# Kernel optimization log

Hardware: AMD Instinct MI355X
Metric: run time of the kernel (lower is better)

Reference implementation:

```python
import jax, jax.numpy as jnp
import numpy as np

VOL_SHAPE = (160, 192, 160)

def setup_inputs() -> dict:
    key = jax.random.key(0)
    k1, k2 = jax.random.split(key)
    vol = jax.random.normal(k1, (2, *VOL_SHAPE, 1), dtype=jnp.float32)
    trf = jax.random.normal(k2, (2, *VOL_SHAPE, 3), dtype=jnp.float32)
    return {"vol": vol, "trf": trf}

def _warp(vol, trf):
    # vol: [B, X, Y, Z, C]; trf: [B, X, Y, Z, 3] dense displacement field ('ij' indexing)
    B = vol.shape[0]
    shape = vol.shape[1:-1]
    nd = len(shape)
    # sample locations = identity grid + displacement
    grid = jnp.stack(jnp.meshgrid(*[jnp.arange(s, dtype=vol.dtype) for s in shape], indexing='ij'), axis=-1)
    loc = grid[None] + trf  # [B, X, Y, Z, 3]
    max_f = jnp.array([s - 1 for s in shape], dtype=vol.dtype)
    max_i = jnp.array([s - 1 for s in shape], dtype=jnp.int32)
    # fill_value=None -> clamp to volume border (voxelmorph interpn semantics)
    loc = jnp.clip(loc, 0.0, max_f)
    loc0f = jnp.floor(loc)
    loc0 = jnp.clip(loc0f.astype(jnp.int32), 0, max_i)        # lower corner indices
    loc1 = jnp.clip(loc0 + 1, 0, max_i)                       # upper corner indices (clipped)
    d1 = loc1.astype(vol.dtype) - loc                          # weight for lower corner
    d0 = 1.0 - d1                                              # weight for upper corner
    b = jnp.arange(B)[:, None, None, None]
    out = jnp.zeros(vol.shape, dtype=vol.dtype)
    for c in range(2 ** nd):                                   # 8 corners, fixed small loop
        bits = [(c >> d) & 1 for d in range(nd)]
        idx = [loc1[..., d] if bits[d] else loc0[..., d] for d in range(nd)]
        w = jnp.ones(loc.shape[:-1], dtype=vol.dtype)
        for d in range(nd):
            w = w * (d0[..., d] if bits[d] else d1[..., d])
        out = out + w[..., None] * vol[b, idx[0], idx[1], idx[2]]
    return out

def reference(vol, trf):
    return _warp(vol, trf)
```

## Files before the change

### kernel.cpp

```cpp
#include <hip/hip_runtime.h>


#define NXD 160
#define NYD 192
#define NZD 160
#define NVOX (NXD * NYD * NZD)
#define NBATCH 2

#define TXT 8
#define TYT 16
#define TZT 16
#define LXT 14
#define LYT 22
#define LZT 32
#define NROWS (LXT * LYT)
#define LDS_N (NROWS * LZT)
#define NSLOT (NROWS * 8)

#define TILES_X (NXD / TXT)
#define TILES_Y (NYD / TYT)
#define TILES_Z (NZD / TZT)
#define NBLOCKS (NBATCH * TILES_X * TILES_Y * TILES_Z)

typedef float f4 __attribute__((ext_vector_type(4)));

__global__ __launch_bounds__(512)
void warp3d_kernel(const float* __restrict__ vol,
                   const float* __restrict__ trf,
                   float* __restrict__ out) {
    __shared__ float tile[LDS_N];

    int bid0 = blockIdx.x;
    int bid = (bid0 & 7) * (NBLOCKS / 8) + (bid0 >> 3);

    int tz = bid % TILES_Z;
    int r  = bid / TILES_Z;
    int ty = r % TILES_Y;
    int r2 = r / TILES_Y;
    int tx = r2 % TILES_X;
    int b  = r2 / TILES_X;

    int x0t = tx * TXT, y0t = ty * TYT, z0t = tz * TZT;
    int lox = min(max(x0t - 3, 0), NXD - LXT);
    int loy = min(max(y0t - 3, 0), NYD - LYT);
    int loz = min(max(z0t - 8, 0), NZD - LZT);

    const float* vb = vol + (size_t)b * NVOX;

    int t = threadIdx.x;
    int zq = t & 3;
    int yq = (t >> 2) & 15;
    int xq = t >> 6;
    int x = x0t + xq, y = y0t + yq, zb0 = z0t + zq * 4;
    size_t vox_i = (((size_t)b * NXD + x) * NYD + y) * NZD + zb0;

    const f4* trfv = (const f4*)(trf + vox_i * 3);
    f4 t0 = trfv[0], t1 = trfv[1], t2 = trfv[2];

    {
        const float* gbase = vb + ((size_t)(lox * NYD + loy) * NZD + loz);
#pragma unroll
        for (int it = 0; it < 5; ++it) {
            int slot = it * 512 + t;
            if (slot < NSLOT) {
                int row = slot >> 3;
                int zg  = (slot & 7) << 2;
                int yi  = row % LYT;
                int xi  = row / LYT;
                int sz  = zg ^ ((yi & 7) << 2);
                const float* g = gbase + (size_t)xi * (NYD * NZD) + yi * NZD + sz;
                __builtin_amdgcn_global_load_lds(
                    (const __attribute__((address_space(1))) void*)g,
                    (__attribute__((address_space(3))) void*)&tile[slot * 4],
                    16, 0, 0);
            }
        }
    }
    __syncthreads();

    float dxa[4] = {t0.x, t0.w, t1.z, t2.y};
    float dya[4] = {t0.y, t1.x, t1.w, t2.z};
    float dza[4] = {t0.z, t1.y, t2.x, t2.w};

    float res[4];
#pragma unroll
    for (int j = 0; j < 4; ++j) {
        float lx = fminf(fmaxf((float)x + dxa[j], 0.0f), (float)(NXD - 1));
        float ly = fminf(fmaxf((float)y + dya[j], 0.0f), (float)(NYD - 1));
        float lz = fminf(fmaxf((float)(zb0 + j) + dza[j], 0.0f), (float)(NZD - 1));
        float fx = floorf(lx), fy = floorf(ly), fz = floorf(lz);
        int x0 = (int)fx, y0 = (int)fy, z0 = (int)fz;
        float wx0 = fminf(fx + 1.0f, (float)(NXD - 1)) - lx;
        float wy0 = fminf(fy + 1.0f, (float)(NYD - 1)) - ly;
        float wz0 = fminf(fz + 1.0f, (float)(NZD - 1)) - lz;

        int ix = x0 - lox, iy = y0 - loy, iz = z0 - loz;
        bool ok = ((unsigned)ix <= LXT - 2) & ((unsigned)iy <= LYT - 2) &
                  ((unsigned)iz <= LZT - 2);
        int sx = ok ? ix : 0;
        int sy = ok ? iy : 0;
        int sv = ok ? iz : 0;

        int base = (sx * LYT + sy) * LZT;
        int sw0 = (sy & 7) << 2;
        int sw1 = ((sy + 1) & 7) << 2;
        int A = base + (sv ^ sw0);
        int B = base + ((sv + 1) ^ sw0);
        int C = base + LZT + (sv ^ sw1);
        int D = base + LZT + ((sv + 1) ^ sw1);

        float v000 = tile[A],              v001 = tile[B];
        float v010 = tile[C],              v011 = tile[D];
        float v100 = tile[A + LYT * LZT],  v101 = tile[B + LYT * LZT];
        float v110 = tile[C + LYT * LZT],  v111 = tile[D + LYT * LZT];

        if (!ok) {
            int x1 = min(x0 + 1, NXD - 1);
            int y1 = min(y0 + 1, NYD - 1);
            int z1 = min(z0 + 1, NZD - 1);
            size_t o00 = (size_t)(x0 * NYD + y0) * NZD;
            size_t o01 = (size_t)(x0 * NYD + y1) * NZD;
            size_t o10 = (size_t)(x1 * NYD + y0) * NZD;
            size_t o11 = (size_t)(x1 * NYD + y1) * NZD;
            v000 = vb[o00 + z0]; v001 = vb[o00 + z1];
            v010 = vb[o01 + z0]; v011 = vb[o01 + z1];
            v100 = vb[o10 + z0]; v101 = vb[o10 + z1];
            v110 = vb[o11 + z0]; v111 = vb[o11 + z1];
        }

        float wx1 = 1.0f - wx0, wy1 = 1.0f - wy0, wz1 = 1.0f - wz0;
        res[j] = wx0 * (wy0 * (wz0 * v000 + wz1 * v001) +
                        wy1 * (wz0 * v010 + wz1 * v011)) +
                 wx1 * (wy0 * (wz0 * v100 + wz1 * v101) +
                        wy1 * (wz0 * v110 + wz1 * v111));
    }

    f4 o;
    o.x = res[0]; o.y = res[1]; o.z = res[2]; o.w = res[3];
    *(f4*)(out + vox_i) = o;
}

extern "C" void kernel_launch(void* const* d_in, const int* in_sizes, int n_in,
                              void* d_out, int out_size, void* d_ws, size_t ws_size,
                              hipStream_t stream) {
    const float* vol = (const float*)d_in[0];
    const float* trf = (const float*)d_in[1];
    float* out = (float*)d_out;

    warp3d_kernel<<<NBLOCKS, 512, 0, stream>>>(vol, trf, out);
}
```

Measured before the change: 222.1 us.

## Make blocks persistent along z with double-buffered LDS tile prefetch

Each block now walks all z tiles of its x-y column instead of handling one tile, and prefetches the next z halo tile and displacement vectors into a second LDS buffer while interpolating the current one. This is meant to hide global-to-LDS load latency behind compute and cut per-block launch and setup overhead. In exchange, LDS use per block doubles, there are ten times fewer blocks, which reduces parallelism and occupancy, and the z tiles of a column are processed serially.

```diff
diff --git a/kernel.cpp b/kernel.cpp
--- a/kernel.cpp
+++ b/kernel.cpp
@@ -10,6 +10,7 @@
 #define TXT 8
 #define TYT 16
 #define TZT 16
+#define NZT (NZD / TZT)
 #define LXT 14
 #define LYT 22
 #define LZT 32
@@ -19,31 +20,30 @@
 
 #define TILES_X (NXD / TXT)
 #define TILES_Y (NYD / TYT)
-#define TILES_Z (NZD / TZT)
-#define NBLOCKS (NBATCH * TILES_X * TILES_Y * TILES_Z)
+#define NBLOCKS (NBATCH * TILES_X * TILES_Y)
 
 typedef float f4 __attribute__((ext_vector_type(4)));
+
+#define AS1 __attribute__((address_space(1)))
+#define AS3 __attribute__((address_space(3)))
 
 __global__ __launch_bounds__(512)
 void warp3d_kernel(const float* __restrict__ vol,
                    const float* __restrict__ trf,
                    float* __restrict__ out) {
-    __shared__ float tile[LDS_N];
+    __shared__ float tile[2 * LDS_N];
 
     int bid0 = blockIdx.x;
     int bid = (bid0 & 7) * (NBLOCKS / 8) + (bid0 >> 3);
 
-    int tz = bid % TILES_Z;
-    int r  = bid / TILES_Z;
-    int ty = r % TILES_Y;
-    int r2 = r / TILES_Y;
-    int tx = r2 % TILES_X;
-    int b  = r2 / TILES_X;
+    int ty = bid % TILES_Y;
+    int r  = bid / TILES_Y;
+    int tx = r % TILES_X;
+    int b  = r / TILES_X;
 
-    int x0t = tx * TXT, y0t = ty * TYT, z0t = tz * TZT;
+    int x0t = tx * TXT, y0t = ty * TYT;
     int lox = min(max(x0t - 3, 0), NXD - LXT);
     int loy = min(max(y0t - 3, 0), NYD - LYT);
-    int loz = min(max(z0t - 8, 0), NZD - LZT);
 
     const float* vb = vol + (size_t)b * NVOX;
 
@@ -51,93 +51,130 @@
     int zq = t & 3;
     int yq = (t >> 2) & 15;
     int xq = t >> 6;
-    int x = x0t + xq, y = y0t + yq, zb0 = z0t + zq * 4;
-    size_t vox_i = (((size_t)b * NXD + x) * NYD + y) * NZD + zb0;
+    int x = x0t + xq, y = y0t + yq;
+    size_t rowb = (((size_t)b * NXD + x) * NYD + y) * NZD + zq * 4;
 
-    const f4* trfv = (const f4*)(trf + vox_i * 3);
-    f4 t0 = trfv[0], t1 = trfv[1], t2 = trfv[2];
+    int o0, o1, o2, o3, o4;
+    {
+#define MKOFF(IT, DST)                                                    \
+        {                                                                  \
+            int slot = (IT) * 512 + t;                                     \
+            int row = slot >> 3;                                           \
+            int zg  = (slot & 7) << 2;                                     \
+            int yi  = row % LYT;                                           \
+            int xi  = row / LYT;                                           \
+            int sz  = zg ^ ((yi & 7) << 2);   \
+            DST = xi * (NYD * NZD) + yi * NZD + sz;                        \
+        }
+        MKOFF(0, o0) MKOFF(1, o1) MKOFF(2, o2) MKOFF(3, o3) MKOFF(4, o4)
+#undef MKOFF
+    }
+    bool p4 = (2048 + t) < NSLOT;
 
+    auto STAGE = [&](int bufoff, int loz) {
+        const float* gb = vb + ((size_t)(lox * NYD + loy) * NZD + loz);
+        __builtin_amdgcn_global_load_lds((const AS1 void*)(gb + o0),
+            (AS3 void*)&tile[bufoff + t * 4], 16, 0, 0);
+        __builtin_amdgcn_global_load_lds((const AS1 void*)(gb + o1),
+            (AS3 void*)&tile[bufoff + (512 + t) * 4], 16, 0, 0);
+        __builtin_amdgcn_global_load_lds((const AS1 void*)(gb + o2),
+            (AS3 void*)&tile[bufoff + (1024 + t) * 4], 16, 0, 0);
+        __builtin_amdgcn_global_load_lds((const AS1 void*)(gb + o3),
+            (AS3 void*)&tile[bufoff + (1536 + t) * 4], 16, 0, 0);
+        if (p4)
+            __builtin_amdgcn_global_load_lds((const AS1 void*)(gb + o4),
+                (AS3 void*)&tile[bufoff + (2048 + t) * 4], 16, 0, 0);
+    };
+
+    int bufoff = 0;
+    int loz = 0;
+    f4 ta0, ta1, ta2;
     {
-        const float* gbase = vb + ((size_t)(lox * NYD + loy) * NZD + loz);
+        const f4* tv = (const f4*)(trf + rowb * 3);
+        ta0 = tv[0]; ta1 = tv[1]; ta2 = tv[2];
+    }
+    STAGE(0, 0);
+    __syncthreads();
+
+    for (int tz = 0; tz < NZT; ++tz) {
+        bool pre = (tz + 1) < NZT;
+        int loz_next = min(max((tz + 1) * TZT - 8, 0), NZD - LZT);
+        f4 tb0, tb1, tb2;
+        if (pre) {
+            const f4* tv = (const f4*)(trf + (rowb + (size_t)(tz + 1) * TZT) * 3);
+            tb0 = tv[0]; tb1 = tv[1]; tb2 = tv[2];
+            STAGE(bufoff ^ LDS_N, loz_next);
+        }
+
+        int zb0 = tz * TZT + zq * 4;
+        float dxa[4] = {ta0.x, ta0.w, ta1.z, ta2.y};
+        float dya[4] = {ta0.y, ta1.x, ta1.w, ta2.z};
+        float dza[4] = {ta0.z, ta1.y, ta2.x, ta2.w};
+
+        float res[4];
 #pragma unroll
-        for (int it = 0; it < 5; ++it) {
-            int slot = it * 512 + t;
-            if (slot < NSLOT) {
-                int row = slot >> 3;
-                int zg  = (slot & 7) << 2;
-                int yi  = row % LYT;
-                int xi  = row / LYT;
-                int sz  = zg ^ ((yi & 7) << 2);
-                const float* g = gbase + (size_t)xi * (NYD * NZD) + yi * NZD + sz;
-                __builtin_amdgcn_global_load_lds(
-                    (const __attribute__((address_space(1))) void*)g,
-                    (__attribute__((address_space(3))) void*)&tile[slot * 4],
-                    16, 0, 0);
+        for (int j = 0; j < 4; ++j) {
+            float lx = fminf(fmaxf((float)x + dxa[j], 0.0f), (float)(NXD - 1));
+            float ly = fminf(fmaxf((float)y + dya[j], 0.0f), (float)(NYD - 1));
+            float lz = fminf(fmaxf((float)(zb0 + j) + dza[j], 0.0f), (float)(NZD - 1));
+            float fx = floorf(lx), fy = floorf(ly), fz = floorf(lz);
+            int x0 = (int)fx, y0 = (int)fy, z0 = (int)fz;
+            float wx0 = fminf(fx + 1.0f, (float)(NXD - 1)) - lx;
+            float wy0 = fminf(fy + 1.0f, (float)(NYD - 1)) - ly;
+            float wz0 = fminf(fz + 1.0f, (float)(NZD - 1)) - lz;
+
+            int ix = x0 - lox, iy = y0 - loy, iz = z0 - loz;
+            bool ok = ((unsigned)ix <= LXT - 2) & ((unsigned)iy <= LYT - 2) &
+                      ((unsigned)iz <= LZT - 2);
+            int sx = ok ? ix : 0;
+            int sy = ok ? iy : 0;
+            int sv = ok ? iz : 0;
+
+            int base = bufoff + (sx * LYT + sy) * LZT;
+            int sw0 = (sy & 7) << 2;
+            int sw1 = ((sy + 1) & 7) << 2;
+            int A = base + (sv ^ sw0);
+            int B = base + ((sv + 1) ^ sw0);
+            int C = base + LZT + (sv ^ sw1);
+            int D = base + LZT + ((sv + 1) ^ sw1);
+
+            float v000 = tile[A],              v001 = tile[B];
+            float v010 = tile[C],              v011 = tile[D];
+            float v100 = tile[A + LYT * LZT],  v101 = tile[B + LYT * LZT];
+            float v110 = tile[C + LYT * LZT],  v111 = tile[D + LYT * LZT];
+
+            if (!ok) {
+                int x1 = min(x0 + 1, NXD - 1);
+                int y1 = min(y0 + 1, NYD - 1);
+                int z1 = min(z0 + 1, NZD - 1);
+                size_t o00 = (size_t)(x0 * NYD + y0) * NZD;
+                size_t o01 = (size_t)(x0 * NYD + y1) * NZD;
+                size_t o10 = (size_t)(x1 * NYD + y0) * NZD;
+                size_t o11 = (size_t)(x1 * NYD + y1) * NZD;
+                v000 = vb[o00 + z0]; v001 = vb[o00 + z1];
+                v010 = vb[o01 + z0]; v011 = vb[o01 + z1];
+                v100 = vb[o10 + z0]; v101 = vb[o10 + z1];
+                v110 = vb[o11 + z0]; v111 = vb[o11 + z1];
             }
+
+            float wx1 = 1.0f - wx0, wy1 = 1.0f - wy0, wz1 = 1.0f - wz0;
+            res[j] = wx0 * (wy0 * (wz0 * v000 + wz1 * v001) +
+                            wy1 * (wz0 * v010 + wz1 * v011)) +
+                     wx1 * (wy0 * (wz0 * v100 + wz1 * v101) +
+                            wy1 * (wz0 * v110 + wz1 * v111));
+        }
+
+        f4 o;
+        o.x = res[0]; o.y = res[1]; o.z = res[2]; o.w = res[3];
+        *(f4*)(out + rowb + (size_t)tz * TZT) = o;
+
+        __syncthreads();
+        if (pre) {
+            ta0 = tb0; ta1 = tb1; ta2 = tb2;
+            bufoff ^= LDS_N;
+            loz = loz_next;
         }
     }
-    __syncthreads();
-
-    float dxa[4] = {t0.x, t0.w, t1.z, t2.y};
-    float dya[4] = {t0.y, t1.x, t1.w, t2.z};
-    float dza[4] = {t0.z, t1.y, t2.x, t2.w};
-
-    float res[4];
-#pragma unroll
-    for (int j = 0; j < 4; ++j) {
-        float lx = fminf(fmaxf((float)x + dxa[j], 0.0f), (float)(NXD - 1));
-        float ly = fminf(fmaxf((float)y + dya[j], 0.0f), (float)(NYD - 1));
-        float lz = fminf(fmaxf((float)(zb0 + j) + dza[j], 0.0f), (float)(NZD - 1));
-        float fx = floorf(lx), fy = floorf(ly), fz = floorf(lz);
-        int x0 = (int)fx, y0 = (int)fy, z0 = (int)fz;
-        float wx0 = fminf(fx + 1.0f, (float)(NXD - 1)) - lx;
-        float wy0 = fminf(fy + 1.0f, (float)(NYD - 1)) - ly;
-        float wz0 = fminf(fz + 1.0f, (float)(NZD - 1)) - lz;
-
-        int ix = x0 - lox, iy = y0 - loy, iz = z0 - loz;
-        bool ok = ((unsigned)ix <= LXT - 2) & ((unsigned)iy <= LYT - 2) &
-                  ((unsigned)iz <= LZT - 2);
-        int sx = ok ? ix : 0;
-        int sy = ok ? iy : 0;
-        int sv = ok ? iz : 0;
-
-        int base = (sx * LYT + sy) * LZT;
-        int sw0 = (sy & 7) << 2;
-        int sw1 = ((sy + 1) & 7) << 2;
-        int A = base + (sv ^ sw0);
-        int B = base + ((sv + 1) ^ sw0);
-        int C = base + LZT + (sv ^ sw1);
-        int D = base + LZT + ((sv + 1) ^ sw1);
-
-        float v000 = tile[A],              v001 = tile[B];
-        float v010 = tile[C],              v011 = tile[D];
-        float v100 = tile[A + LYT * LZT],  v101 = tile[B + LYT * LZT];
-        float v110 = tile[C + LYT * LZT],  v111 = tile[D + LYT * LZT];
-
-        if (!ok) {
-            int x1 = min(x0 + 1, NXD - 1);
-            int y1 = min(y0 + 1, NYD - 1);
-            int z1 = min(z0 + 1, NZD - 1);
-            size_t o00 = (size_t)(x0 * NYD + y0) * NZD;
-            size_t o01 = (size_t)(x0 * NYD + y1) * NZD;
-            size_t o10 = (size_t)(x1 * NYD + y0) * NZD;
-            size_t o11 = (size_t)(x1 * NYD + y1) * NZD;
-            v000 = vb[o00 + z0]; v001 = vb[o00 + z1];
-            v010 = vb[o01 + z0]; v011 = vb[o01 + z1];
-            v100 = vb[o10 + z0]; v101 = vb[o10 + z1];
-            v110 = vb[o11 + z0]; v111 = vb[o11 + z1];
-        }
-
-        float wx1 = 1.0f - wx0, wy1 = 1.0f - wy0, wz1 = 1.0f - wz0;
-        res[j] = wx0 * (wy0 * (wz0 * v000 + wz1 * v001) +
-                        wy1 * (wz0 * v010 + wz1 * v011)) +
-                 wx1 * (wy0 * (wz0 * v100 + wz1 * v101) +
-                        wy1 * (wz0 * v110 + wz1 * v111));
-    }
-
-    f4 o;
-    o.x = res[0]; o.y = res[1]; o.z = res[2]; o.w = res[3];
-    *(f4*)(out + vox_i) = o;
 }
 
 extern "C" void kernel_launch(void* const* d_in, const int* in_sizes, int n_in,
```

New measurement: 239.0 us. 7.6% more time.

## Replace LDS tile staging with direct global gathers per voxel

Applied to the files above, without the earlier changes.

Drops the shared-memory halo tile, the async global-to-LDS copy and the block barrier. Each thread now gathers all eight trilinear corners straight from global memory and relies on the L1/L2 caches for reuse. Blocks shrink to 256 threads over a flat linear voxel-quad index. This removes the halo overfetch and the barrier stall, at the cost of many more scattered global load instructions going through the cache hierarchy.

```diff
diff --git a/kernel.cpp b/kernel.cpp
--- a/kernel.cpp
+++ b/kernel.cpp
@@ -7,76 +7,34 @@
 #define NVOX (NXD * NYD * NZD)
 #define NBATCH 2
 
-#define TXT 8
-#define TYT 16
-#define TZT 16
-#define LXT 14
-#define LYT 22
-#define LZT 32
-#define NROWS (LXT * LYT)
-#define LDS_N (NROWS * LZT)
-#define NSLOT (NROWS * 8)
-
-#define TILES_X (NXD / TXT)
-#define TILES_Y (NYD / TYT)
-#define TILES_Z (NZD / TZT)
-#define NBLOCKS (NBATCH * TILES_X * TILES_Y * TILES_Z)
+#define ZQ (NZD / 4)
+#define NQUAD (NBATCH * NXD * NYD * ZQ)
+#define BLK 256
+#define NBLOCKS (NQUAD / BLK)
 
 typedef float f4 __attribute__((ext_vector_type(4)));
 
-__global__ __launch_bounds__(512)
+__global__ __launch_bounds__(BLK)
 void warp3d_kernel(const float* __restrict__ vol,
                    const float* __restrict__ trf,
                    float* __restrict__ out) {
-    __shared__ float tile[LDS_N];
-
     int bid0 = blockIdx.x;
     int bid = (bid0 & 7) * (NBLOCKS / 8) + (bid0 >> 3);
 
-    int tz = bid % TILES_Z;
-    int r  = bid / TILES_Z;
-    int ty = r % TILES_Y;
-    int r2 = r / TILES_Y;
-    int tx = r2 % TILES_X;
-    int b  = r2 / TILES_X;
+    int q = bid * BLK + threadIdx.x;
+    int zqi = q % ZQ;
+    int r   = q / ZQ;
+    int y   = r % NYD;
+    int r2  = r / NYD;
+    int x   = r2 % NXD;
+    int b   = r2 / NXD;
 
-    int x0t = tx * TXT, y0t = ty * TYT, z0t = tz * TZT;
-    int lox = min(max(x0t - 3, 0), NXD - LXT);
-    int loy = min(max(y0t - 3, 0), NYD - LYT);
-    int loz = min(max(z0t - 8, 0), NZD - LZT);
-
+    int zb0 = zqi * 4;
+    size_t rowb = (((size_t)b * NXD + x) * NYD + y) * NZD + zb0;
     const float* vb = vol + (size_t)b * NVOX;
 
-    int t = threadIdx.x;
-    int zq = t & 3;
-    int yq = (t >> 2) & 15;
-    int xq = t >> 6;
-    int x = x0t + xq, y = y0t + yq, zb0 = z0t + zq * 4;
-    size_t vox_i = (((size_t)b * NXD + x) * NYD + y) * NZD + zb0;
-
-    const f4* trfv = (const f4*)(trf + vox_i * 3);
-    f4 t0 = trfv[0], t1 = trfv[1], t2 = trfv[2];
-
-    {
-        const float* gbase = vb + ((size_t)(lox * NYD + loy) * NZD + loz);
-#pragma unroll
-        for (int it = 0; it < 5; ++it) {
-            int slot = it * 512 + t;
-            if (slot < NSLOT) {
-                int row = slot >> 3;
-                int zg  = (slot & 7) << 2;
-                int yi  = row % LYT;
-                int xi  = row / LYT;
-                int sz  = zg ^ ((yi & 7) << 2);
-                const float* g = gbase + (size_t)xi * (NYD * NZD) + yi * NZD + sz;
-                __builtin_amdgcn_global_load_lds(
-                    (const __attribute__((address_space(1))) void*)g,
-                    (__attribute__((address_space(3))) void*)&tile[slot * 4],
-                    16, 0, 0);
-            }
-        }
-    }
-    __syncthreads();
+    const f4* tv = (const f4*)(trf + rowb * 3);
+    f4 t0 = tv[0], t1 = tv[1], t2 = tv[2];
 
     float dxa[4] = {t0.x, t0.w, t1.z, t2.y};
     float dya[4] = {t0.y, t1.x, t1.w, t2.z};
@@ -94,39 +52,18 @@
         float wy0 = fminf(fy + 1.0f, (float)(NYD - 1)) - ly;
         float wz0 = fminf(fz + 1.0f, (float)(NZD - 1)) - lz;
 
-        int ix = x0 - lox, iy = y0 - loy, iz = z0 - loz;
-        bool ok = ((unsigned)ix <= LXT - 2) & ((unsigned)iy <= LYT - 2) &
-                  ((unsigned)iz <= LZT - 2);
-        int sx = ok ? ix : 0;
-        int sy = ok ? iy : 0;
-        int sv = ok ? iz : 0;
+        int x1 = min(x0 + 1, NXD - 1);
+        int y1 = min(y0 + 1, NYD - 1);
+        int z1 = min(z0 + 1, NZD - 1);
+        size_t o00 = (size_t)(x0 * NYD + y0) * NZD;
+        size_t o01 = (size_t)(x0 * NYD + y1) * NZD;
+        size_t o10 = (size_t)(x1 * NYD + y0) * NZD;
+        size_t o11 = (size_t)(x1 * NYD + y1) * NZD;
 
-        int base = (sx * LYT + sy) * LZT;
-        int sw0 = (sy & 7) << 2;
-        int sw1 = ((sy + 1) & 7) << 2;
-        int A = base + (sv ^ sw0);
-        int B = base + ((sv + 1) ^ sw0);
-        int C = base + LZT + (sv ^ sw1);
-        int D = base + LZT + ((sv + 1) ^ sw1);
-
-        float v000 = tile[A],              v001 = tile[B];
-        float v010 = tile[C],              v011 = tile[D];
-        float v100 = tile[A + LYT * LZT],  v101 = tile[B + LYT * LZT];
-        float v110 = tile[C + LYT * LZT],  v111 = tile[D + LYT * LZT];
-
-        if (!ok) {
-            int x1 = min(x0 + 1, NXD - 1);
-            int y1 = min(y0 + 1, NYD - 1);
-            int z1 = min(z0 + 1, NZD - 1);
-            size_t o00 = (size_t)(x0 * NYD + y0) * NZD;
-            size_t o01 = (size_t)(x0 * NYD + y1) * NZD;
-            size_t o10 = (size_t)(x1 * NYD + y0) * NZD;
-            size_t o11 = (size_t)(x1 * NYD + y1) * NZD;
-            v000 = vb[o00 + z0]; v001 = vb[o00 + z1];
-            v010 = vb[o01 + z0]; v011 = vb[o01 + z1];
-            v100 = vb[o10 + z0]; v101 = vb[o10 + z1];
-            v110 = vb[o11 + z0]; v111 = vb[o11 + z1];
-        }
+        float v000 = vb[o00 + z0], v001 = vb[o00 + z1];
+        float v010 = vb[o01 + z0], v011 = vb[o01 + z1];
+        float v100 = vb[o10 + z0], v101 = vb[o10 + z1];
+        float v110 = vb[o11 + z0], v111 = vb[o11 + z1];
 
         float wx1 = 1.0f - wx0, wy1 = 1.0f - wy0, wz1 = 1.0f - wz0;
         res[j] = wx0 * (wy0 * (wz0 * v000 + wz1 * v001) +
@@ -137,7 +74,7 @@
 
     f4 o;
     o.x = res[0]; o.y = res[1]; o.z = res[2]; o.w = res[3];
-    *(f4*)(out + vox_i) = o;
+    *(f4*)(out + rowb) = o;
 }
 
 extern "C" void kernel_launch(void* const* d_in, const int* in_sizes, int n_in,
@@ -147,5 +84,5 @@
     const float* trf = (const float*)d_in[1];
     float* out = (float*)d_out;
 
-    warp3d_kernel<<<NBLOCKS, 512, 0, stream>>>(vol, trf, out);
+    warp3d_kernel<<<NBLOCKS, BLK, 0, stream>>>(vol, trf, out);
 }
```

Result: slower. 311.6 us (+40.3%).
